# Optimization experiments

Hardware: AMD Instinct MI355X
Metric: run time of the kernel (lower is better)

Reference implementation:

```python
import jax, jax.numpy as jnp
import numpy as np

B, L, H, O, C = 64, 32, 128, 16384, 32


def setup_inputs() -> dict:
    key = jax.random.key(0)
    ks = jax.random.split(key, 8)
    s = lambda k, shp, fan: jax.random.normal(k, shp, jnp.float32) / np.sqrt(fan)
    return {
        "z": jax.random.normal(ks[0], (B, L), jnp.float32),
        "feature_embedding": jax.random.normal(ks[1], (O, C), jnp.float32),
        "feature_bias": jax.random.normal(ks[2], (O, 1), jnp.float32),
        "Wz": s(ks[3], (L, H), L),
        "bz": jnp.zeros((H,), jnp.float32),
        "W1": s(ks[4], (H + C + 1, H), H + C + 1),
        "b1": jnp.zeros((H,), jnp.float32),
        "W2": s(ks[5], (H, 1), H),
        "b2": jnp.zeros((1,), jnp.float32),
    }


def reference(z, feature_embedding, feature_bias, Wz, bz, W1, b1, W2, b2):
    # z_processor: Linear + ReLU (dropout_rate=0)
    pz = jax.nn.relu(z @ Wz + bz)  # [B, H]
    # concat([pz, F, b], -1) @ W1  ==  pz@W1_h + F@W1_f + b*W1_b  (no [B,O,H+C+1] materialization)
    W1_h, W1_f, W1_b = W1[:H], W1[H:H + C], W1[H + C:]  # [H,H],[C,H],[1,H]
    h = jax.nn.relu(
        (pz @ W1_h)[:, None, :]                    # [B,1,H]
        + (feature_embedding @ W1_f)[None, :, :]   # [1,O,H]
        + feature_bias * W1_b                      # [O,H] broadcast
        + b1
    )  # [B, O, H]
    out = jnp.einsum("boh,ho->bo", h, W2) + b2  # [B, O]
    return out
```

## Files before the change

kernel.cpp:

```cpp
#include <hip/hip_runtime.h>

#define Bb 64
#define Ll 32
#define Hh 128
#define Oo 16384
#define Cc 32
#define TOo 64
#define NT 1024

__global__ __launch_bounds__(256) void prep_kernel(
    const float* __restrict__ z, const float* __restrict__ Wz,
    const float* __restrict__ bz, const float* __restrict__ W1,
    const float* __restrict__ W2,
    float* __restrict__ A, float* __restrict__ SA2w)
{
    __shared__ float pz[2][Hh];
    __shared__ float ps[2][Hh];
    const int t  = threadIdx.x;
    const int h  = t & (Hh - 1);
    const int bb = t >> 7;
    const int b  = blockIdx.x * 2 + bb;

    float v = bz[h];
#pragma unroll
    for (int c = 0; c < Ll; ++c)
        v = fmaf(z[b * Ll + c], Wz[c * Hh + h], v);
    pz[bb][h] = fmaxf(v, 0.f);
    __syncthreads();

    float a = 0.f;
#pragma unroll
    for (int k = 0; k < Hh; ++k)
        a = fmaf(pz[bb][k], W1[k * Hh + h], a);
    A[b * Hh + h] = a;
    ps[bb][h] = 0.5f * W2[h] * a;
    __syncthreads();

    if (h == 0) {
        float s = 0.f;
        for (int k = 0; k < Hh; ++k) s += ps[bb][k];
        SA2w[b] = s;
    }
}

__global__ __launch_bounds__(NT) void main_kernel(
    const float* __restrict__ A,  const float* __restrict__ SA2w,
    const float* __restrict__ fe, const float* __restrict__ fb,
    const float* __restrict__ W1, const float* __restrict__ b1,
    const float* __restrict__ W2, const float* __restrict__ b2,
    float* __restrict__ out)
{
    __shared__ float fe_s[TOo][Cc];
    __shared__ float gT[Hh][TOo + 1];
    __shared__ float A_s[Bb][Hh];
    __shared__ float part[4][Bb][TOo];
    __shared__ float w2_s[Hh];
    __shared__ float fb_s[TOo];

    const int t  = threadIdx.x;
    const int o0 = blockIdx.x * TOo;

    if (t < 512) ((float4*)fe_s)[t] = ((const float4*)(fe + o0 * Cc))[t];
    ((float4*)A_s)[t]        = ((const float4*)A)[t];
    ((float4*)A_s)[t + 1024] = ((const float4*)A)[t + 1024];
    if (t < Hh)  w2_s[t] = 0.5f * W2[t];
    if (t < TOo) fb_s[t] = fb[o0 + t];
    const float b2v = b2[0];
    __syncthreads();

    {
        const int h  = t & 127;
        const int og = t >> 7;
        float w1f[Cc];
#pragma unroll
        for (int c = 0; c < Cc; ++c)
            w1f[c] = W1[(Hh + c) * Hh + h];
        const float w1b = W1[(Hh + Cc) * Hh + h];
        const float b1h = b1[h];
#pragma unroll
        for (int j = 0; j < 8; ++j) {
            const int o = og * 8 + j;
            float g = fmaf(fb_s[o], w1b, b1h);
#pragma unroll
            for (int cc = 0; cc < Cc / 4; ++cc) {
                const float4 f4 = ((const float4*)fe_s[o])[cc];
                g = fmaf(f4.x, w1f[4 * cc + 0], g);
                g = fmaf(f4.y, w1f[4 * cc + 1], g);
                g = fmaf(f4.z, w1f[4 * cc + 2], g);
                g = fmaf(f4.w, w1f[4 * cc + 3], g);
            }
            gT[h][o] = g;
        }
    }
    __syncthreads();

    const int lane = t & 63;
    const int wave = __builtin_amdgcn_readfirstlane(t >> 6);
    const int hh   = wave & 3;
    const int bg   = wave >> 2;
    const int h0   = hh * 32;
    const int b0   = bg * 16;

    float gv[32];
#pragma unroll
    for (int k = 0; k < 32; ++k)
        gv[k] = gT[h0 + k][lane];

    float w2v[32];
#pragma unroll
    for (int k = 0; k < 8; ++k) {
        const float4 w4 = ((const float4*)(w2_s + h0))[k];
        w2v[4 * k + 0] = w4.x; w2v[4 * k + 1] = w4.y;
        w2v[4 * k + 2] = w4.z; w2v[4 * k + 3] = w4.w;
    }

    float sg = 0.f;
#pragma unroll
    for (int k = 0; k < 32; ++k)
        sg = fmaf(w2v[k], gv[k], sg);

    float acc[16];
#pragma unroll
    for (int bi = 0; bi < 16; ++bi) acc[bi] = sg;

#pragma unroll
    for (int jc = 0; jc < 8; ++jc) {
#pragma unroll
        for (int bi = 0; bi < 16; ++bi) {
            const float4 a4 = *(const float4*)&A_s[b0 + bi][h0 + 4 * jc];
            acc[bi] = fmaf(__builtin_fabsf(a4.x + gv[4 * jc + 0]), w2v[4 * jc + 0], acc[bi]);
            acc[bi] = fmaf(__builtin_fabsf(a4.y + gv[4 * jc + 1]), w2v[4 * jc + 1], acc[bi]);
            acc[bi] = fmaf(__builtin_fabsf(a4.z + gv[4 * jc + 2]), w2v[4 * jc + 2], acc[bi]);
            acc[bi] = fmaf(__builtin_fabsf(a4.w + gv[4 * jc + 3]), w2v[4 * jc + 3], acc[bi]);
        }
    }

#pragma unroll
    for (int bi = 0; bi < 16; ++bi)
        part[hh][b0 + bi][lane] = acc[bi];
    __syncthreads();

#pragma unroll
    for (int q = 0; q < 4; ++q) {
        const int b = wave * 4 + q;
        const float r = part[0][b][lane] + part[1][b][lane]
                      + part[2][b][lane] + part[3][b][lane];
        out[b * Oo + o0 + lane] = r + SA2w[b] + b2v;
    }
}

extern "C" void kernel_launch(void* const* d_in, const int* in_sizes, int n_in,
                              void* d_out, int out_size, void* d_ws, size_t ws_size,
                              hipStream_t stream) {
    (void)in_sizes; (void)n_in; (void)out_size; (void)ws_size;
    const float* z   = (const float*)d_in[0];
    const float* fe  = (const float*)d_in[1];
    const float* fb  = (const float*)d_in[2];
    const float* Wz  = (const float*)d_in[3];
    const float* bz  = (const float*)d_in[4];
    const float* W1  = (const float*)d_in[5];
    const float* b1  = (const float*)d_in[6];
    const float* W2  = (const float*)d_in[7];
    const float* b2  = (const float*)d_in[8];
    float* out  = (float*)d_out;
    float* A    = (float*)d_ws;
    float* SA2w = A + Bb * Hh;

    prep_kernel<<<Bb / 2, 256, 0, stream>>>(z, Wz, bz, W1, W2, A, SA2w);
    main_kernel<<<Oo / TOo, NT, 0, stream>>>(A, SA2w, fe, fb, W1, b1, W2, b2, out);
}
```

Before: 87.58 us.

## Use packed fp16 with fdot2 for the inner abs-sum and feature projection

Converts A, the feature embeddings, W1_f, the per-output g values and W2 to packed half2 and computes both the feature projection and the |a+g|*w2 accumulation with v_dot2 (fdot2) into fp32 accumulators. This halves the number of inner-loop instructions and the LDS footprint and traffic for A and fe. In exchange it rounds the intermediates to fp16, which lowers accuracy and may exceed the tolerance.

```diff
diff --git a/kernel.cpp b/kernel.cpp
--- a/kernel.cpp
+++ b/kernel.cpp
@@ -1,4 +1,5 @@
 #include <hip/hip_runtime.h>
+#include <hip/hip_fp16.h>
 
 #define Bb 64
 #define Ll 32
@@ -8,13 +9,28 @@
 #define TOo 64
 #define NT 1024
 
+typedef _Float16 h2 __attribute__((ext_vector_type(2)));
+
+static __device__ __forceinline__ unsigned pk_rn(float x, float y) {
+    unsigned short ux = __half_as_ushort(__float2half_rn(x));
+    unsigned short uy = __half_as_ushort(__float2half_rn(y));
+    return (unsigned)ux | ((unsigned)uy << 16);
+}
+static __device__ __forceinline__ h2 as_h2(unsigned u) {
+    union { unsigned u; h2 h; } v; v.u = u; return v.h;
+}
+static __device__ __forceinline__ h2 habs2(h2 x) {
+    union { h2 h; unsigned u; } v; v.h = x; v.u &= 0x7FFF7FFFu; return v.h;
+}
+
 __global__ __launch_bounds__(256) void prep_kernel(
     const float* __restrict__ z, const float* __restrict__ Wz,
     const float* __restrict__ bz, const float* __restrict__ W1,
     const float* __restrict__ W2,
-    float* __restrict__ A, float* __restrict__ SA2w)
+    unsigned* __restrict__ A16, float* __restrict__ SA2w)
 {
     __shared__ float pz[2][Hh];
+    __shared__ float af[2][Hh];
     __shared__ float ps[2][Hh];
     const int t  = threadIdx.x;
     const int h  = t & (Hh - 1);
@@ -32,9 +48,12 @@
 #pragma unroll
     for (int k = 0; k < Hh; ++k)
         a = fmaf(pz[bb][k], W1[k * Hh + h], a);
-    A[b * Hh + h] = a;
+    af[bb][h] = a;
     ps[bb][h] = 0.5f * W2[h] * a;
     __syncthreads();
+
+    if (h < Hh / 2)
+        A16[b * (Hh / 2) + h] = pk_rn(af[bb][2 * h], af[bb][2 * h + 1]);
 
     if (h == 0) {
         float s = 0.f;
@@ -44,25 +63,30 @@
 }
 
 __global__ __launch_bounds__(NT) void main_kernel(
-    const float* __restrict__ A,  const float* __restrict__ SA2w,
+    const unsigned* __restrict__ A16, const float* __restrict__ SA2w,
     const float* __restrict__ fe, const float* __restrict__ fb,
     const float* __restrict__ W1, const float* __restrict__ b1,
     const float* __restrict__ W2, const float* __restrict__ b2,
     float* __restrict__ out)
 {
-    __shared__ float fe_s[TOo][Cc];
-    __shared__ float gT[Hh][TOo + 1];
-    __shared__ float A_s[Bb][Hh];
-    __shared__ float part[4][Bb][TOo];
-    __shared__ float w2_s[Hh];
-    __shared__ float fb_s[TOo];
+    __shared__ unsigned fe_h[TOo][Cc / 2];
+    __shared__ float    gT[Hh][TOo + 1];
+    __shared__ unsigned A_h[Bb][Hh / 2];
+    __shared__ float    part[4][Bb][TOo];
+    __shared__ float    w2_s[Hh];
+    __shared__ float    fb_s[TOo];
 
     const int t  = threadIdx.x;
     const int o0 = blockIdx.x * TOo;
 
-    if (t < 512) ((float4*)fe_s)[t] = ((const float4*)(fe + o0 * Cc))[t];
-    ((float4*)A_s)[t]        = ((const float4*)A)[t];
-    ((float4*)A_s)[t + 1024] = ((const float4*)A)[t + 1024];
+    if (t < 512) {
+        const float4 f4 = ((const float4*)(fe + o0 * Cc))[t];
+        uint2 p;
+        p.x = pk_rn(f4.x, f4.y);
+        p.y = pk_rn(f4.z, f4.w);
+        ((uint2*)fe_h)[t] = p;
+    }
+    ((uint4*)A_h)[t] = ((const uint4*)A16)[t];
     if (t < Hh)  w2_s[t] = 0.5f * W2[t];
     if (t < TOo) fb_s[t] = fb[o0 + t];
     const float b2v = b2[0];
@@ -71,23 +95,27 @@
     {
         const int h  = t & 127;
         const int og = t >> 7;
-        float w1f[Cc];
-#pragma unroll
-        for (int c = 0; c < Cc; ++c)
-            w1f[c] = W1[(Hh + c) * Hh + h];
+        h2 w1f2[Cc / 2];
+#pragma unroll
+        for (int cc = 0; cc < Cc / 2; ++cc) {
+            const float x = W1[(Hh + 2 * cc) * Hh + h];
+            const float y = W1[(Hh + 2 * cc + 1) * Hh + h];
+            w1f2[cc] = as_h2(pk_rn(x, y));
+        }
         const float w1b = W1[(Hh + Cc) * Hh + h];
         const float b1h = b1[h];
 #pragma unroll
         for (int j = 0; j < 8; ++j) {
             const int o = og * 8 + j;
             float g = fmaf(fb_s[o], w1b, b1h);
-#pragma unroll
-            for (int cc = 0; cc < Cc / 4; ++cc) {
-                const float4 f4 = ((const float4*)fe_s[o])[cc];
-                g = fmaf(f4.x, w1f[4 * cc + 0], g);
-                g = fmaf(f4.y, w1f[4 * cc + 1], g);
-                g = fmaf(f4.z, w1f[4 * cc + 2], g);
-                g = fmaf(f4.w, w1f[4 * cc + 3], g);
+            const uint4* q4 = (const uint4*)&fe_h[o][0];
+#pragma unroll
+            for (int cc = 0; cc < 4; ++cc) {
+                const uint4 q = q4[cc];
+                g = __builtin_amdgcn_fdot2(as_h2(q.x), w1f2[4 * cc + 0], g, false);
+                g = __builtin_amdgcn_fdot2(as_h2(q.y), w1f2[4 * cc + 1], g, false);
+                g = __builtin_amdgcn_fdot2(as_h2(q.z), w1f2[4 * cc + 2], g, false);
+                g = __builtin_amdgcn_fdot2(as_h2(q.w), w1f2[4 * cc + 3], g, false);
             }
             gT[h][o] = g;
         }
@@ -101,37 +129,48 @@
     const int h0   = hh * 32;
     const int b0   = bg * 16;
 
-    float gv[32];
+    float gvf[32];
 #pragma unroll
     for (int k = 0; k < 32; ++k)
-        gv[k] = gT[h0 + k][lane];
-
-    float w2v[32];
+        gvf[k] = gT[h0 + k][lane];
+
+    float w2f[32];
 #pragma unroll
     for (int k = 0; k < 8; ++k) {
         const float4 w4 = ((const float4*)(w2_s + h0))[k];
-        w2v[4 * k + 0] = w4.x; w2v[4 * k + 1] = w4.y;
-        w2v[4 * k + 2] = w4.z; w2v[4 * k + 3] = w4.w;
+        w2f[4 * k + 0] = w4.x; w2f[4 * k + 1] = w4.y;
+        w2f[4 * k + 2] = w4.z; w2f[4 * k + 3] = w4.w;
     }
 
     float sg = 0.f;
 #pragma unroll
     for (int k = 0; k < 32; ++k)
-        sg = fmaf(w2v[k], gv[k], sg);
+        sg = fmaf(w2f[k], gvf[k], sg);
+
+    h2 g2[16], w22[16];
+#pragma unroll
+    for (int k = 0; k < 16; ++k) {
+        g2[k]  = as_h2(pk_rn(gvf[2 * k], gvf[2 * k + 1]));
+        w22[k] = as_h2(pk_rn(w2f[2 * k], w2f[2 * k + 1]));
+    }
 
     float acc[16];
 #pragma unroll
     for (int bi = 0; bi < 16; ++bi) acc[bi] = sg;
 
 #pragma unroll
-    for (int jc = 0; jc < 8; ++jc) {
+    for (int jc = 0; jc < 4; ++jc) {
 #pragma unroll
         for (int bi = 0; bi < 16; ++bi) {
-            const float4 a4 = *(const float4*)&A_s[b0 + bi][h0 + 4 * jc];
-            acc[bi] = fmaf(__builtin_fabsf(a4.x + gv[4 * jc + 0]), w2v[4 * jc + 0], acc[bi]);
-            acc[bi] = fmaf(__builtin_fabsf(a4.y + gv[4 * jc + 1]), w2v[4 * jc + 1], acc[bi]);
-            acc[bi] = fmaf(__builtin_fabsf(a4.z + gv[4 * jc + 2]), w2v[4 * jc + 2], acc[bi]);
-            acc[bi] = fmaf(__builtin_fabsf(a4.w + gv[4 * jc + 3]), w2v[4 * jc + 3], acc[bi]);
+            const uint4 a4 = *(const uint4*)&A_h[b0 + bi][hh * 16 + 4 * jc];
+            acc[bi] = __builtin_amdgcn_fdot2(habs2(as_h2(a4.x) + g2[4 * jc + 0]),
+                                             w22[4 * jc + 0], acc[bi], false);
+            acc[bi] = __builtin_amdgcn_fdot2(habs2(as_h2(a4.y) + g2[4 * jc + 1]),
+                                             w22[4 * jc + 1], acc[bi], false);
+            acc[bi] = __builtin_amdgcn_fdot2(habs2(as_h2(a4.z) + g2[4 * jc + 2]),
+                                             w22[4 * jc + 2], acc[bi], false);
+            acc[bi] = __builtin_amdgcn_fdot2(habs2(as_h2(a4.w) + g2[4 * jc + 3]),
+                                             w22[4 * jc + 3], acc[bi], false);
         }
     }
 
@@ -162,10 +201,10 @@
     const float* b1  = (const float*)d_in[6];
     const float* W2  = (const float*)d_in[7];
     const float* b2  = (const float*)d_in[8];
-    float* out  = (float*)d_out;
-    float* A    = (float*)d_ws;
-    float* SA2w = A + Bb * Hh;
-
-    prep_kernel<<<Bb / 2, 256, 0, stream>>>(z, Wz, bz, W1, W2, A, SA2w);
-    main_kernel<<<Oo / TOo, NT, 0, stream>>>(A, SA2w, fe, fb, W1, b1, W2, b2, out);
-}
+    float* out       = (float*)d_out;
+    unsigned* A16    = (unsigned*)d_ws;
+    float* SA2w      = (float*)(A16 + Bb * (Hh / 2));
+
+    prep_kernel<<<Bb / 2, 256, 0, stream>>>(z, Wz, bz, W1, W2, A16, SA2w);
+    main_kernel<<<Oo / TOo, NT, 0, stream>>>(A16, SA2w, fe, fb, W1, b1, W2, b2, out);
+}
```

After: 84.38 us. 3.7% less time.
